# Kernel tuning notes

Measured on AMD Instinct MI355X. Metric: run time of the kernel, lower is better.

The kernel has to match this reference:

```python
import jax, jax.numpy as jnp
import numpy as np

TEMP = 0.1
EPS = 1e-9  # torch CosineSimilarity eps


def setup_inputs() -> dict:
    key = jax.random.key(0)
    k1, k2 = jax.random.split(key)
    h = jax.random.normal(k1, (16384, 2048), dtype=jnp.float32)
    W = jax.random.normal(k2, (512, 2048), dtype=jnp.float32) * (1.0 / np.sqrt(2048))
    return {"h": h, "W": W}


def reference(h, W):
    # process_reps: h already 2D -> identity. Split into anchor / context halves.
    B = h.shape[0] // 2
    wz = h[:B] @ W.T      # [B, low_rank_dim]
    wc = h[B:] @ W.T      # [B, low_rank_dim]

    # CosineSimilarity(dim=-1, eps=1e-9): dot / max(||z||*||c||, eps), pairwise BxB
    nz = jnp.linalg.norm(wz, axis=-1)  # [B]
    nc = jnp.linalg.norm(wc, axis=-1)  # [B]
    sim = (wz @ wc.T) / jnp.maximum(nz[:, None] * nc[None, :], EPS)  # [B, B]
    sim = sim / TEMP

    sim_mean = sim.mean()
    sim_pos = jnp.diagonal(sim).mean()
    logprob = -jax.nn.log_softmax(sim, axis=1)
    loss = jnp.diagonal(logprob).mean()
    # matches loss_dict entries: {'loss', 'loss_pos', 'loss_neg'}
    return jnp.stack([loss, sim_pos, sim_mean])
```

## Files before the change

### kernel.cpp

```cpp
#include <hip/hip_runtime.h>


typedef __attribute__((ext_vector_type(8))) short bf16x8;
typedef __attribute__((ext_vector_type(4))) float floatx4;
typedef unsigned char uchar;

__device__ __forceinline__ unsigned short f2bf(float f) {
    union { float f; unsigned u; } v; v.f = f;
    unsigned r = (v.u + 0x7FFFu + ((v.u >> 16) & 1u)) >> 16;
    return (unsigned short)r;
}

__device__ __forceinline__ void async_copy16(const void* g, void* l) {
    __builtin_amdgcn_global_load_lds(
        (const __attribute__((address_space(1))) void*)g,
        (__attribute__((address_space(3))) void*)l,
        16, 0, 0);
}

__global__ __launch_bounds__(256) void cast_fp8_kernel(
    const float* __restrict__ src, uchar* __restrict__ dst, int n, float scale)
{
    const int i = (blockIdx.x * 256 + threadIdx.x) * 8;
    if (i + 7 < n) {
        float4 a = *reinterpret_cast<const float4*>(src + i);
        float4 b = *reinterpret_cast<const float4*>(src + i + 4);
        const int p01 = __builtin_amdgcn_cvt_pk_fp8_f32(a.x * scale, a.y * scale, 0, 0);
        const int p23 = __builtin_amdgcn_cvt_pk_fp8_f32(a.z * scale, a.w * scale, 0, 0);
        const int p45 = __builtin_amdgcn_cvt_pk_fp8_f32(b.x * scale, b.y * scale, 0, 0);
        const int p67 = __builtin_amdgcn_cvt_pk_fp8_f32(b.z * scale, b.w * scale, 0, 0);
        int2 w;
        w.x = (p01 & 0xffff) | (p23 << 16);
        w.y = (p45 & 0xffff) | (p67 << 16);
        *reinterpret_cast<int2*>(dst + i) = w;
    }
}

__device__ __forceinline__ size_t fl_off(int row_g, int col_g) {
    const int g = row_g >> 4, r15 = row_g & 15;
    const int c = col_g >> 5, q = (col_g >> 3) & 3, b = col_g & 7;
    return ((size_t)g * 16 + c) * 512 + (size_t)(q * 16 + r15) * 8 + b;
}

__global__ __launch_bounds__(256, 2) void g1f(
    const float* __restrict__ h, const uchar* __restrict__ W8,
    uchar* __restrict__ Z8F, float* __restrict__ norm2)
{
    __shared__ __align__(16) uchar As[64 * 64];
    __shared__ __align__(16) uchar Bs[512 * 64];

    const int blk = blockIdx.x;
    const int t = threadIdx.x;
    const int wave = t >> 6, lane = t & 63;
    const int quad = lane >> 4, l15 = lane & 15;

    floatx4 acc[32];
    #pragma unroll
    for (int j = 0; j < 32; j++) acc[j] = {0.f, 0.f, 0.f, 0.f};

    const int arow = t >> 2, ap = t & 3;
    const float* gH = h + (size_t)(blk * 64 + arow) * 2048 + ap * 16;
    uchar* lA = &As[arow * 64 + ((ap ^ ((arow >> 1) & 3)) << 4)];

    const int brow0 = wave * 128 + (lane >> 2);
    const int bswz = ((lane & 3) ^ ((brow0 >> 1) & 3)) << 4;
    const uchar* gB = W8 + (size_t)brow0 * 2048 + bswz;
    uchar* lB = &Bs[wave * 128 * 64];

    const int swzr = (l15 >> 1) & 3;
    const int arow_r = wave * 16 + l15;

    float4 f0 = *reinterpret_cast<const float4*>(gH + 0);
    float4 f1 = *reinterpret_cast<const float4*>(gH + 4);
    float4 f2 = *reinterpret_cast<const float4*>(gH + 8);
    float4 f3 = *reinterpret_cast<const float4*>(gH + 12);

    for (int k0 = 0; k0 < 2048; k0 += 64) {
        #pragma unroll
        for (int s = 0; s < 8; s++)
            async_copy16(gB + k0 + s * 32768, lB + s * 1024);
        {
            const int p01 = __builtin_amdgcn_cvt_pk_fp8_f32(f0.x, f0.y, 0, 0);
            const int p23 = __builtin_amdgcn_cvt_pk_fp8_f32(f0.z, f0.w, 0, 0);
            const int p45 = __builtin_amdgcn_cvt_pk_fp8_f32(f1.x, f1.y, 0, 0);
            const int p67 = __builtin_amdgcn_cvt_pk_fp8_f32(f1.z, f1.w, 0, 0);
            const int p89 = __builtin_amdgcn_cvt_pk_fp8_f32(f2.x, f2.y, 0, 0);
            const int pAB = __builtin_amdgcn_cvt_pk_fp8_f32(f2.z, f2.w, 0, 0);
            const int pCD = __builtin_amdgcn_cvt_pk_fp8_f32(f3.x, f3.y, 0, 0);
            const int pEF = __builtin_amdgcn_cvt_pk_fp8_f32(f3.z, f3.w, 0, 0);
            int4 pk;
            pk.x = (p01 & 0xffff) | (p23 << 16);
            pk.y = (p45 & 0xffff) | (p67 << 16);
            pk.z = (p89 & 0xffff) | (pAB << 16);
            pk.w = (pCD & 0xffff) | (pEF << 16);
            *reinterpret_cast<int4*>(lA) = pk;
        }
        __syncthreads();

        if (k0 < 2048 - 64) {
            f0 = *reinterpret_cast<const float4*>(gH + k0 + 64);
            f1 = *reinterpret_cast<const float4*>(gH + k0 + 68);
            f2 = *reinterpret_cast<const float4*>(gH + k0 + 72);
            f3 = *reinterpret_cast<const float4*>(gH + k0 + 76);
        }

        #pragma unroll
        for (int ch = 0; ch < 2; ch++) {
            const int s = ch * 2 + (quad >> 1);
            const int sub = (quad & 1) * 8;
            const int phys = ((s ^ swzr) << 4) + sub;
            const long a = *reinterpret_cast<const long*>(&As[arow_r * 64 + phys]);
            #pragma unroll
            for (int jg = 0; jg < 4; jg++) {
                long bb[8];
                #pragma unroll
                for (int u = 0; u < 8; u++) {
                    const int brow = (jg * 8 + u) * 16 + l15;
                    bb[u] = *reinterpret_cast<const long*>(&Bs[brow * 64 + phys]);
                }
                __builtin_amdgcn_s_setprio(1);
                #pragma unroll
                for (int u = 0; u < 8; u++)
                    acc[jg * 8 + u] = __builtin_amdgcn_mfma_f32_16x16x32_fp8_fp8(
                        a, bb[u], acc[jg * 8 + u], 0, 0, 0);
                __builtin_amdgcn_s_setprio(0);
            }
        }
        __syncthreads();
    }

    #pragma unroll
    for (int r = 0; r < 4; r++) {
        const int row_g = blk * 64 + wave * 16 + quad * 4 + r;
        float pw = 0.f;
        #pragma unroll
        for (int jp = 0; jp < 16; jp++) {
            const int pk = __builtin_amdgcn_cvt_pk_fp8_f32(
                acc[2 * jp][r], acc[2 * jp + 1][r], 0, 0);
            Z8F[fl_off(row_g, (2 * jp) * 16 + l15)]     = (uchar)(pk & 0xff);
            Z8F[fl_off(row_g, (2 * jp + 1) * 16 + l15)] = (uchar)((pk >> 8) & 0xff);
            const float q0 = __builtin_amdgcn_cvt_f32_fp8(pk, 0);
            const float q1 = __builtin_amdgcn_cvt_f32_fp8(pk, 1);
            pw += q0 * q0 + q1 * q1;
        }
        pw += __shfl_xor(pw, 1, 16);
        pw += __shfl_xor(pw, 2, 16);
        pw += __shfl_xor(pw, 4, 16);
        pw += __shfl_xor(pw, 8, 16);
        if (l15 == 0) norm2[row_g] = pw;
    }
}

__global__ __launch_bounds__(256) void g1_slow(
    const float* __restrict__ h, const float* __restrict__ W,
    uchar* __restrict__ Z8F, float* __restrict__ norm2)
{
    __shared__ __align__(16) unsigned short As[128][40];
    __shared__ __align__(16) unsigned short Bs[128][40];

    const int bn = blockIdx.x, bm = blockIdx.y;
    const int t = threadIdx.x;
    const int wave = t >> 6, lane = t & 63;
    const int wm = wave & 1, wn = wave >> 1;
    const int quad = lane >> 4, l15 = lane & 15;

    floatx4 acc[4][4];
    #pragma unroll
    for (int i = 0; i < 4; i++)
        #pragma unroll
        for (int j = 0; j < 4; j++) acc[i][j] = {0.f, 0.f, 0.f, 0.f};

    const int lrow = t >> 1, lhalf = t & 1;
    const float* ga = h + (size_t)(bm * 128 + lrow) * 2048 + lhalf * 16;
    const float* gb = W + (size_t)(bn * 128 + lrow) * 2048 + lhalf * 16;

    for (int k0 = 0; k0 < 2048; k0 += 32) {
        #pragma unroll
        for (int c = 0; c < 4; c++) {
            const float4 va = *reinterpret_cast<const float4*>(ga + k0 + c * 4);
            const float4 vb = *reinterpret_cast<const float4*>(gb + k0 + c * 4);
            ushort4 ua = make_ushort4(f2bf(va.x), f2bf(va.y), f2bf(va.z), f2bf(va.w));
            ushort4 ub = make_ushort4(f2bf(vb.x), f2bf(vb.y), f2bf(vb.z), f2bf(vb.w));
            *reinterpret_cast<ushort4*>(&As[lrow][lhalf * 16 + c * 4]) = ua;
            *reinterpret_cast<ushort4*>(&Bs[lrow][lhalf * 16 + c * 4]) = ub;
        }
        __syncthreads();
        bf16x8 af[4], bfr[4];
        #pragma unroll
        for (int i = 0; i < 4; i++)
            af[i] = *reinterpret_cast<const bf16x8*>(&As[wm * 64 + i * 16 + l15][quad * 8]);
        #pragma unroll
        for (int j = 0; j < 4; j++)
            bfr[j] = *reinterpret_cast<const bf16x8*>(&Bs[wn * 64 + j * 16 + l15][quad * 8]);
        #pragma unroll
        for (int i = 0; i < 4; i++)
            #pragma unroll
            for (int j = 0; j < 4; j++)
                acc[i][j] = __builtin_amdgcn_mfma_f32_16x16x32_bf16(af[i], bfr[j], acc[i][j], 0, 0, 0);
        __syncthreads();
    }

    #pragma unroll
    for (int i = 0; i < 4; i++) {
        #pragma unroll
        for (int r = 0; r < 4; r++) {
            const int row_g = bm * 128 + wm * 64 + i * 16 + quad * 4 + r;
            const int pk01 = __builtin_amdgcn_cvt_pk_fp8_f32(acc[i][0][r], acc[i][1][r], 0, 0);
            const int pk23 = __builtin_amdgcn_cvt_pk_fp8_f32(acc[i][2][r], acc[i][3][r], 0, 0);
            const uchar q8[4] = { (uchar)(pk01 & 0xff), (uchar)((pk01 >> 8) & 0xff),
                                  (uchar)(pk23 & 0xff), (uchar)((pk23 >> 8) & 0xff) };
            #pragma unroll
            for (int j = 0; j < 4; j++) {
                const int col_g = bn * 128 + wn * 64 + j * 16 + l15;
                Z8F[fl_off(row_g, col_g)] = q8[j];
            }
            const float q0 = __builtin_amdgcn_cvt_f32_fp8(pk01, 0);
            const float q1 = __builtin_amdgcn_cvt_f32_fp8(pk01, 1);
            const float q2 = __builtin_amdgcn_cvt_f32_fp8(pk23, 0);
            const float q3 = __builtin_amdgcn_cvt_f32_fp8(pk23, 1);
            float pw = q0 * q0 + q1 * q1 + q2 * q2 + q3 * q3;
            pw += __shfl_xor(pw, 1, 16);
            pw += __shfl_xor(pw, 2, 16);
            pw += __shfl_xor(pw, 4, 16);
            pw += __shfl_xor(pw, 8, 16);
            if (l15 == 0) atomicAdd(&norm2[row_g], pw);
        }
    }
}

__global__ __launch_bounds__(256, 4) void g2_main(
    const uchar* __restrict__ Z8F, const float* __restrict__ norm2,
    float* __restrict__ rowse, float* __restrict__ bsum, float* __restrict__ bdiag)
{
    __shared__ __align__(16) uchar Bs[32768];
    __shared__ float red[8];
    float (*lds_red)[20] = (float (*)[20])(void*)Bs;

    const int o = blockIdx.y * 64 + blockIdx.x;
    const int xcd = o & 7, idx = o >> 3;
    const int bg = idx >> 7, r = idx & 127;
    const int bm = xcd * 8 + (r >> 4);
    const int bn = bg * 16 + (r & 15);
    const int t = threadIdx.x;
    const int wave = t >> 6, lane = t & 63;
    const int quad = lane >> 4, l15 = lane & 15;

    const uchar* gB = Z8F + (size_t)(512 + bn * 8) * 8192 + t * 16;
    #pragma unroll
    for (int s = 0; s < 8; s++)
        async_copy16(gB + s * 8192, &Bs[s * 4096 + wave * 1024]);

    floatx4 acc[2][8];
    #pragma unroll
    for (int i = 0; i < 2; i++)
        #pragma unroll
        for (int j = 0; j < 8; j++) acc[i][j] = {0.f, 0.f, 0.f, 0.f};

    const uchar* baseA = Z8F + (size_t)(bm * 8 + wave * 2) * 8192 + lane * 8;

    long ab[3][2];
    #pragma unroll
    for (int d = 0; d < 2; d++)
        #pragma unroll
        for (int i = 0; i < 2; i++)
            ab[d][i] = *reinterpret_cast<const long*>(baseA + i * 8192 + d * 512);

    __syncthreads();

    #pragma unroll
    for (int c = 0; c < 16; c++) {
        const int cl = c & 7;
        if (c < 14) {
            #pragma unroll
            for (int i = 0; i < 2; i++)
                ab[(c + 2) % 3][i] = *reinterpret_cast<const long*>(
                    baseA + i * 8192 + (c + 2) * 512);
        }
        long bb[8];
        #pragma unroll
        for (int j = 0; j < 8; j++)
            bb[j] = *reinterpret_cast<const long*>(&Bs[j * 4096 + cl * 512 + lane * 8]);
        __builtin_amdgcn_s_setprio(1);
        #pragma unroll
        for (int i = 0; i < 2; i++)
            #pragma unroll
            for (int j = 0; j < 8; j++)
                acc[i][j] = __builtin_amdgcn_mfma_f32_16x16x32_fp8_fp8(
                    ab[c % 3][i], bb[j], acc[i][j], 0, 0, 0);
        __builtin_amdgcn_s_setprio(0);
        if (c == 7) {
            __syncthreads();
            #pragma unroll
            for (int s = 0; s < 8; s++)
                async_copy16(gB + s * 8192 + 4096, &Bs[s * 4096 + wave * 1024]);
            __syncthreads();
        }
    }

    __syncthreads();

    float rc8[8];
    #pragma unroll
    for (int j = 0; j < 8; j++)
        rc8[j] = rsqrtf(fmaxf(norm2[8192 + bn * 128 + j * 16 + l15], 1e-30f));

    const bool diagblk = (bm == bn);
    float s_tot2 = 0.f, s_diag2 = 0.f;
    #pragma unroll
    for (int i = 0; i < 2; i++) {
        #pragma unroll
        for (int rr = 0; rr < 4; rr++) {
            const int row_t = wave * 32 + i * 16 + quad * 4 + rr;
            const float rzl2 = rsqrtf(fmaxf(norm2[bm * 128 + row_t], 1e-30f)) * 14.4269504089f;
            float rx = 0.f;
            #pragma unroll
            for (int j = 0; j < 8; j++) {
                const float sim2 = acc[i][j][rr] * rzl2 * rc8[j];
                s_tot2 += sim2;
                rx += exp2f(sim2);
                if (diagblk && j == wave * 2 + i && l15 == quad * 4 + rr)
                    s_diag2 += sim2;
            }
            lds_red[row_t][l15] = rx;
        }
    }
    __syncthreads();

    {
        const int row = t >> 1, half = t & 1;
        float v = 0.f;
        #pragma unroll
        for (int cc = 0; cc < 8; cc++) v += lds_red[row][half * 8 + cc];
        v += __shfl_xor(v, 1, 64);
        if (half == 0) atomicAdd(&rowse[bm * 128 + row], v);
    }

    #pragma unroll
    for (int off = 32; off; off >>= 1) {
        s_tot2  += __shfl_xor(s_tot2, off, 64);
        s_diag2 += __shfl_xor(s_diag2, off, 64);
    }
    if (lane == 0) { red[wave] = s_tot2; red[4 + wave] = s_diag2; }
    __syncthreads();
    if (t == 0) {
        bsum[bm * 64 + bn]  = (red[0] + red[1] + red[2] + red[3]) * 0.69314718056f;
        bdiag[bm * 64 + bn] = (red[4] + red[5] + red[6] + red[7]) * 0.69314718056f;
    }
}

__global__ __launch_bounds__(256) void finalize_kernel(
    const float* __restrict__ rowse, const float* __restrict__ bsum,
    const float* __restrict__ bdiag, float* __restrict__ out)
{
    float a = 0.f, b = 0.f, c = 0.f;
    for (int i = threadIdx.x; i < 8192; i += 256) a += logf(rowse[i]);
    for (int i = threadIdx.x; i < 4096; i += 256) { b += bsum[i]; c += bdiag[i]; }
    #pragma unroll
    for (int off = 32; off; off >>= 1) {
        a += __shfl_xor(a, off, 64);
        b += __shfl_xor(b, off, 64);
        c += __shfl_xor(c, off, 64);
    }
    __shared__ float ra[4], rb[4], rc[4];
    const int wave = threadIdx.x >> 6, lane = threadIdx.x & 63;
    if (lane == 0) { ra[wave] = a; rb[wave] = b; rc[wave] = c; }
    __syncthreads();
    if (threadIdx.x == 0) {
        const float A = ra[0] + ra[1] + ra[2] + ra[3];
        const float B = rb[0] + rb[1] + rb[2] + rb[3];
        const float C = rc[0] + rc[1] + rc[2] + rc[3];
        const float diag_mean = C / 8192.f;
        out[0] = A / 8192.f - diag_mean;
        out[1] = diag_mean;
        out[2] = B / (8192.f * 8192.f);
    }
}

extern "C" void kernel_launch(void* const* d_in, const int* in_sizes, int n_in,
                              void* d_out, int out_size, void* d_ws, size_t ws_size,
                              hipStream_t stream) {
    const float* h = (const float*)d_in[0];
    const float* W = (const float*)d_in[1];
    float* out = (float*)d_out;

    char* ws = (char*)d_ws;
    float* norm2 = (float*)(ws);
    float* rowse = (float*)(ws + 65536);
    float* bsum  = (float*)(ws + 98304);
    float* bdiag = (float*)(ws + 114688);
    uchar* Z8F   = (uchar*)(ws + 131072);
    uchar* W8    = (uchar*)(ws + 8519680);
    const size_t NEED_FAST = 9568256ull;

    hipMemsetAsync(ws, 0, 131072, stream);

    if (ws_size >= NEED_FAST) {
        const int nw = 512 * 2048;
        hipLaunchKernelGGL(cast_fp8_kernel, dim3(nw / 2048), dim3(256), 0, stream, W, W8, nw, 32.0f);
        hipLaunchKernelGGL(g1f, dim3(256), dim3(256), 0, stream, h, W8, Z8F, norm2);
    } else {
        hipLaunchKernelGGL(g1_slow, dim3(4, 128), dim3(256), 0, stream, h, W, Z8F, norm2);
    }
    hipLaunchKernelGGL(g2_main, dim3(64, 64), dim3(256), 0, stream, Z8F, norm2, rowse, bsum, bdiag);
    hipLaunchKernelGGL(finalize_kernel, dim3(1), dim3(256), 0, stream, rowse, bsum, bdiag, out);
}
```

Baseline: 285.2 us.

## Double-buffer and software-pipeline the fp8 projection GEMM with a new wave tiling

Rewrites the g1f projection kernel so it uses two LDS buffers for the A and B tiles. Loads and fp8 conversion for step k+1, plus the global prefetch of h for step k+2, are issued after the MFMAs of step k, with explicit vmcnt waits and raw barriers replacing __syncthreads. Each wave now computes a 64x128 output tile instead of 16x512, so every wave holds several A fragments and fewer B fragments per step; the LDS XOR swizzle is dropped. Because each row's squared norm is now split across waves, it is accumulated with atomicAdd, which relies on norm2 being zeroed beforehand. Occupancy drops to one block per CU, and the unswizzled LDS reads may cause bank conflicts.

```diff
diff --git a/kernel.cpp b/kernel.cpp
--- a/kernel.cpp
+++ b/kernel.cpp
@@ -16,6 +16,19 @@
         (const __attribute__((address_space(1))) void*)g,
         (__attribute__((address_space(3))) void*)l,
         16, 0, 0);
+}
+
+__device__ __forceinline__ void cvt16(const float4* f, uchar* dst) {
+    int4 pk;
+    pk.x = (__builtin_amdgcn_cvt_pk_fp8_f32(f[0].x, f[0].y, 0, 0) & 0xffff)
+         | (__builtin_amdgcn_cvt_pk_fp8_f32(f[0].z, f[0].w, 0, 0) << 16);
+    pk.y = (__builtin_amdgcn_cvt_pk_fp8_f32(f[1].x, f[1].y, 0, 0) & 0xffff)
+         | (__builtin_amdgcn_cvt_pk_fp8_f32(f[1].z, f[1].w, 0, 0) << 16);
+    pk.z = (__builtin_amdgcn_cvt_pk_fp8_f32(f[2].x, f[2].y, 0, 0) & 0xffff)
+         | (__builtin_amdgcn_cvt_pk_fp8_f32(f[2].z, f[2].w, 0, 0) << 16);
+    pk.w = (__builtin_amdgcn_cvt_pk_fp8_f32(f[3].x, f[3].y, 0, 0) & 0xffff)
+         | (__builtin_amdgcn_cvt_pk_fp8_f32(f[3].z, f[3].w, 0, 0) << 16);
+    *reinterpret_cast<int4*>(dst) = pk;
 }
 
 __global__ __launch_bounds__(256) void cast_fp8_kernel(
@@ -42,112 +55,113 @@
     return ((size_t)g * 16 + c) * 512 + (size_t)(q * 16 + r15) * 8 + b;
 }
 
-__global__ __launch_bounds__(256, 2) void g1f(
+#define G1F_BODY(K, FC, FN, AR, BR, AW, BW, VM, STAGE_B, STAGE_H)              \
+  {                                                                            \
+    asm volatile("s_waitcnt vmcnt(" #VM ")" ::: "memory");                     \
+    asm volatile("s_waitcnt lgkmcnt(0)" ::: "memory");                         \
+    __builtin_amdgcn_s_barrier();                                              \
+    __builtin_amdgcn_sched_barrier(0);                                         \
+    long av[2][4], bv[2][8];                                                   \
+    _Pragma("unroll")                                                          \
+    for (int c = 0; c < 2; c++) {                                              \
+      _Pragma("unroll")                                                        \
+      for (int i = 0; i < 4; i++)                                              \
+        av[c][i] = *reinterpret_cast<const long*>(AR + fA + i * 1024 + c * 32);\
+      _Pragma("unroll")                                                        \
+      for (int j = 0; j < 8; j++)                                              \
+        bv[c][j] = *reinterpret_cast<const long*>(BR + fB + j * 1024 + c * 32);\
+    }                                                                          \
+    __builtin_amdgcn_s_setprio(1);                                             \
+    _Pragma("unroll")                                                          \
+    for (int c = 0; c < 2; c++)                                                \
+      _Pragma("unroll")                                                        \
+      for (int i = 0; i < 4; i++)                                              \
+        _Pragma("unroll")                                                      \
+        for (int j = 0; j < 8; j++)                                            \
+          acc[i][j] = __builtin_amdgcn_mfma_f32_16x16x32_fp8_fp8(              \
+              av[c][i], bv[c][j], acc[i][j], 0, 0, 0);                         \
+    __builtin_amdgcn_s_setprio(0);                                             \
+    if (STAGE_B) {                                                             \
+      _Pragma("unroll")                                                        \
+      for (int s = 0; s < 8; s++)                                              \
+        async_copy16(gBs + ((K) + 1) * 64 + s * 131072, BW + swave + s * 4096);\
+      cvt16(FC, AW + aoff);                                                    \
+    }                                                                          \
+    if (STAGE_H) {                                                             \
+      _Pragma("unroll")                                                        \
+      for (int c4 = 0; c4 < 4; c4++)                                           \
+        FN[c4] = *reinterpret_cast<const float4*>(gH + ((K) + 2) * 64 + c4 * 4);\
+    }                                                                          \
+  }
+
+__global__ __launch_bounds__(256, 1) void g1f(
     const float* __restrict__ h, const uchar* __restrict__ W8,
     uchar* __restrict__ Z8F, float* __restrict__ norm2)
 {
-    __shared__ __align__(16) uchar As[64 * 64];
-    __shared__ __align__(16) uchar Bs[512 * 64];
+    __shared__ __align__(16) uchar As0[64 * 64],  As1[64 * 64];
+    __shared__ __align__(16) uchar Bs0[512 * 64], Bs1[512 * 64];
 
     const int blk = blockIdx.x;
     const int t = threadIdx.x;
     const int wave = t >> 6, lane = t & 63;
     const int quad = lane >> 4, l15 = lane & 15;
 
-    floatx4 acc[32];
-    #pragma unroll
-    for (int j = 0; j < 32; j++) acc[j] = {0.f, 0.f, 0.f, 0.f};
+    floatx4 acc[4][8];
+    #pragma unroll
+    for (int i = 0; i < 4; i++)
+        #pragma unroll
+        for (int j = 0; j < 8; j++) acc[i][j] = {0.f, 0.f, 0.f, 0.f};
 
     const int arow = t >> 2, ap = t & 3;
     const float* gH = h + (size_t)(blk * 64 + arow) * 2048 + ap * 16;
-    uchar* lA = &As[arow * 64 + ((ap ^ ((arow >> 1) & 3)) << 4)];
-
-    const int brow0 = wave * 128 + (lane >> 2);
-    const int bswz = ((lane & 3) ^ ((brow0 >> 1) & 3)) << 4;
-    const uchar* gB = W8 + (size_t)brow0 * 2048 + bswz;
-    uchar* lB = &Bs[wave * 128 * 64];
-
-    const int swzr = (l15 >> 1) & 3;
-    const int arow_r = wave * 16 + l15;
-
-    float4 f0 = *reinterpret_cast<const float4*>(gH + 0);
-    float4 f1 = *reinterpret_cast<const float4*>(gH + 4);
-    float4 f2 = *reinterpret_cast<const float4*>(gH + 8);
-    float4 f3 = *reinterpret_cast<const float4*>(gH + 12);
-
-    for (int k0 = 0; k0 < 2048; k0 += 64) {
-        #pragma unroll
-        for (int s = 0; s < 8; s++)
-            async_copy16(gB + k0 + s * 32768, lB + s * 1024);
-        {
-            const int p01 = __builtin_amdgcn_cvt_pk_fp8_f32(f0.x, f0.y, 0, 0);
-            const int p23 = __builtin_amdgcn_cvt_pk_fp8_f32(f0.z, f0.w, 0, 0);
-            const int p45 = __builtin_amdgcn_cvt_pk_fp8_f32(f1.x, f1.y, 0, 0);
-            const int p67 = __builtin_amdgcn_cvt_pk_fp8_f32(f1.z, f1.w, 0, 0);
-            const int p89 = __builtin_amdgcn_cvt_pk_fp8_f32(f2.x, f2.y, 0, 0);
-            const int pAB = __builtin_amdgcn_cvt_pk_fp8_f32(f2.z, f2.w, 0, 0);
-            const int pCD = __builtin_amdgcn_cvt_pk_fp8_f32(f3.x, f3.y, 0, 0);
-            const int pEF = __builtin_amdgcn_cvt_pk_fp8_f32(f3.z, f3.w, 0, 0);
-            int4 pk;
-            pk.x = (p01 & 0xffff) | (p23 << 16);
-            pk.y = (p45 & 0xffff) | (p67 << 16);
-            pk.z = (p89 & 0xffff) | (pAB << 16);
-            pk.w = (pCD & 0xffff) | (pEF << 16);
-            *reinterpret_cast<int4*>(lA) = pk;
-        }
-        __syncthreads();
-
-        if (k0 < 2048 - 64) {
-            f0 = *reinterpret_cast<const float4*>(gH + k0 + 64);
-            f1 = *reinterpret_cast<const float4*>(gH + k0 + 68);
-            f2 = *reinterpret_cast<const float4*>(gH + k0 + 72);
-            f3 = *reinterpret_cast<const float4*>(gH + k0 + 76);
-        }
-
-        #pragma unroll
-        for (int ch = 0; ch < 2; ch++) {
-            const int s = ch * 2 + (quad >> 1);
-            const int sub = (quad & 1) * 8;
-            const int phys = ((s ^ swzr) << 4) + sub;
-            const long a = *reinterpret_cast<const long*>(&As[arow_r * 64 + phys]);
-            #pragma unroll
-            for (int jg = 0; jg < 4; jg++) {
-                long bb[8];
-                #pragma unroll
-                for (int u = 0; u < 8; u++) {
-                    const int brow = (jg * 8 + u) * 16 + l15;
-                    bb[u] = *reinterpret_cast<const long*>(&Bs[brow * 64 + phys]);
-                }
-                __builtin_amdgcn_s_setprio(1);
-                #pragma unroll
-                for (int u = 0; u < 8; u++)
-                    acc[jg * 8 + u] = __builtin_amdgcn_mfma_f32_16x16x32_fp8_fp8(
-                        a, bb[u], acc[jg * 8 + u], 0, 0, 0);
-                __builtin_amdgcn_s_setprio(0);
+    const int aoff = arow * 64 + ap * 16;
+
+    const uchar* gBs = W8 + (size_t)(wave * 16 + (lane >> 2)) * 2048 + (lane & 3) * 16;
+    const int swave = wave * 1024;
+
+    const int fA = l15 * 64 + quad * 8;
+    const int fB = wave * 8192 + l15 * 64 + quad * 8;
+
+    #pragma unroll
+    for (int s = 0; s < 8; s++)
+        async_copy16(gBs + s * 131072, Bs0 + swave + s * 4096);
+    float4 p0[4], f0[4], f1[4];
+    #pragma unroll
+    for (int c = 0; c < 4; c++) p0[c] = *reinterpret_cast<const float4*>(gH + c * 4);
+    #pragma unroll
+    for (int c = 0; c < 4; c++) f1[c] = *reinterpret_cast<const float4*>(gH + 64 + c * 4);
+    cvt16(p0, As0 + aoff);
+
+    for (int kb = 0; kb < 15; kb++) {
+        const int k = kb * 2;
+        G1F_BODY(k,     f1, f0, As0, Bs0, As1, Bs1, 4, 1, 1)
+        G1F_BODY(k + 1, f0, f1, As1, Bs1, As0, Bs0, 4, 1, 1)
+    }
+    G1F_BODY(30, f1, f0, As0, Bs0, As1, Bs1, 4, 1, 0)
+    G1F_BODY(31, f0, f1, As1, Bs1, As0, Bs0, 0, 0, 0)
+
+    #pragma unroll
+    for (int i = 0; i < 4; i++) {
+        #pragma unroll
+        for (int r = 0; r < 4; r++) {
+            const int row_g = blk * 64 + i * 16 + quad * 4 + r;
+            float pw = 0.f;
+            #pragma unroll
+            for (int jp = 0; jp < 4; jp++) {
+                const int pk = __builtin_amdgcn_cvt_pk_fp8_f32(
+                    acc[i][2 * jp][r], acc[i][2 * jp + 1][r], 0, 0);
+                Z8F[fl_off(row_g, wave * 128 + (2 * jp) * 16 + l15)]     = (uchar)(pk & 0xff);
+                Z8F[fl_off(row_g, wave * 128 + (2 * jp + 1) * 16 + l15)] = (uchar)((pk >> 8) & 0xff);
+                const float q0 = __builtin_amdgcn_cvt_f32_fp8(pk, 0);
+                const float q1 = __builtin_amdgcn_cvt_f32_fp8(pk, 1);
+                pw += q0 * q0 + q1 * q1;
             }
-        }
-        __syncthreads();
-    }
-
-    #pragma unroll
-    for (int r = 0; r < 4; r++) {
-        const int row_g = blk * 64 + wave * 16 + quad * 4 + r;
-        float pw = 0.f;
-        #pragma unroll
-        for (int jp = 0; jp < 16; jp++) {
-            const int pk = __builtin_amdgcn_cvt_pk_fp8_f32(
-                acc[2 * jp][r], acc[2 * jp + 1][r], 0, 0);
-            Z8F[fl_off(row_g, (2 * jp) * 16 + l15)]     = (uchar)(pk & 0xff);
-            Z8F[fl_off(row_g, (2 * jp + 1) * 16 + l15)] = (uchar)((pk >> 8) & 0xff);
-            const float q0 = __builtin_amdgcn_cvt_f32_fp8(pk, 0);
-            const float q1 = __builtin_amdgcn_cvt_f32_fp8(pk, 1);
-            pw += q0 * q0 + q1 * q1;
-        }
-        pw += __shfl_xor(pw, 1, 16);
-        pw += __shfl_xor(pw, 2, 16);
-        pw += __shfl_xor(pw, 4, 16);
-        pw += __shfl_xor(pw, 8, 16);
-        if (l15 == 0) norm2[row_g] = pw;
+            pw += __shfl_xor(pw, 1, 16);
+            pw += __shfl_xor(pw, 2, 16);
+            pw += __shfl_xor(pw, 4, 16);
+            pw += __shfl_xor(pw, 8, 16);
+            if (l15 == 0) atomicAdd(&norm2[row_g], pw);
+        }
     }
 }
 
```

Measured after the change: 317.8 us. 1.11x slower.
